# Kernel tuning notes

Hardware: AMD Instinct MI355X
Metric: run time of the kernel (lower is better)

## Reference

```python
import jax, jax.numpy as jnp
import numpy as np

NUM_HEADS = 12
TOP_K = 2
ROPE_THETA = 10000.0
EPS = 1e-6

def _rmsnorm(x, w):
    return x * jax.lax.rsqrt(jnp.mean(x * x, axis=-1, keepdims=True) + EPS) * w

def _rotate_half(t):
    t1, t2 = jnp.split(t, 2, axis=-1)
    return jnp.concatenate([-t2, t1], axis=-1)

def setup_inputs() -> dict:
    key = jax.random.key(0)
    ks = jax.random.split(key, 8)
    B, S, H, E, F = 2, 2048, 768, 8, 3072
    s = 0.02
    return {
        "x": jax.random.normal(ks[0], (B, S, H), dtype=jnp.float32),
        "attn_norm_w": jnp.ones((H,), dtype=jnp.float32),
        "wqkv": jax.random.normal(ks[1], (H, 3 * H), dtype=jnp.float32) * s,
        "wo": jax.random.normal(ks[2], (H, H), dtype=jnp.float32) * s,
        "ffn_norm_w": jnp.ones((H,), dtype=jnp.float32),
        "router_w": jax.random.normal(ks[3], (H, E), dtype=jnp.float32) * s,
        "w1": jax.random.normal(ks[4], (E, H, F), dtype=jnp.float32) * s,
        "w2": jax.random.normal(ks[5], (E, F, H), dtype=jnp.float32) * s,
    }

def reference(x, attn_norm_w, wqkv, wo, ffn_norm_w, router_w, w1, w2):
    B, S, H = x.shape
    NH, Dh = NUM_HEADS, H // NUM_HEADS
    E = router_w.shape[1]

    # ---- attention sub-block: x = x + attn(rmsnorm(x)) ----
    h = _rmsnorm(x, attn_norm_w)
    qkv = h @ wqkv  # (B,S,3H)
    q, k, v = [t.reshape(B, S, NH, Dh) for t in jnp.split(qkv, 3, axis=-1)]

    # RoPE (llama-style half-split rotation)
    half = Dh // 2
    inv_freq = 1.0 / (ROPE_THETA ** (jnp.arange(half, dtype=jnp.float32) / half))
    ang = jnp.arange(S, dtype=jnp.float32)[:, None] * inv_freq[None, :]  # (S, half)
    cos = jnp.concatenate([jnp.cos(ang)] * 2, axis=-1)[None, :, None, :].astype(x.dtype)
    sin = jnp.concatenate([jnp.sin(ang)] * 2, axis=-1)[None, :, None, :].astype(x.dtype)
    q = q * cos + _rotate_half(q) * sin
    k = k * cos + _rotate_half(k) * sin

    scores = jnp.einsum('bqhd,bkhd->bhqk', q, k) / jnp.sqrt(jnp.asarray(Dh, x.dtype))
    causal = jnp.tril(jnp.ones((S, S), dtype=bool))
    scores = jnp.where(causal[None, None], scores, jnp.asarray(-1e9, x.dtype))
    attn = jax.nn.softmax(scores, axis=-1)
    o = jnp.einsum('bhqk,bkhd->bqhd', attn, v).reshape(B, S, H) @ wo
    x = x + o

    # ---- MoE FFN sub-block: x = x + moe(rmsnorm(x)) ----
    hn = _rmsnorm(x, ffn_norm_w).reshape(-1, H)  # (T,H)
    logits = hn @ router_w  # (T,E)
    probs = jax.nn.softmax(logits, axis=-1)
    top_v, top_i = jax.lax.top_k(probs, TOP_K)  # (T,K)
    top_v = top_v / jnp.sum(top_v, axis=-1, keepdims=True)
    onehot = jax.nn.one_hot(top_i, E, dtype=x.dtype)  # (T,K,E)
    combine = jnp.einsum('tke,tk->te', onehot, top_v)  # (T,E)

    h1 = jnp.einsum('th,ehf->etf', hn, w1)
    h2 = jnp.einsum('etf,efh->eth', jax.nn.silu(h1), w2)
    moe_out = jnp.einsum('eth,te->th', h2, combine).reshape(B, S, H)

    # load-balancing aux loss (switch-style)
    frac = jnp.mean(jnp.sum(onehot, axis=1), axis=0) / TOP_K  # (E,)
    mean_prob = jnp.mean(probs, axis=0)  # (E,)
    aux = jnp.asarray(E, x.dtype) * jnp.sum(frac * mean_prob)

    return (x + moe_out, aux)
```

## Files before the change

kernel.cpp:

```cpp
#include <hip/hip_runtime.h>
#include <cstdint>
#include <cstddef>

typedef __bf16 bf16;
typedef bf16 bf16x8 __attribute__((ext_vector_type(8)));
typedef float f32x4 __attribute__((ext_vector_type(4)));

__device__ __forceinline__ void async_cp16(const void* g, void* l) {
    __builtin_amdgcn_global_load_lds(
        (const __attribute__((address_space(1))) unsigned int*)(unsigned long long)g,
        (__attribute__((address_space(3))) unsigned int*)(unsigned int)(unsigned long long)l,
        16, 0, 0);
}

__global__ __launch_bounds__(256) void transpose_cast(const float* __restrict__ in,
                                                      bf16* __restrict__ out, int R, int C) {
    __shared__ float tile[32][33];
    int bz = blockIdx.z;
    in  += (size_t)bz * R * C;
    out += (size_t)bz * R * C;
    int c0 = blockIdx.x * 32, r0 = blockIdx.y * 32;
    int tx = threadIdx.x & 31, ty = threadIdx.x >> 5;
#pragma unroll
    for (int i = 0; i < 4; ++i)
        tile[ty + i * 8][tx] = in[(size_t)(r0 + ty + i * 8) * C + c0 + tx];
    __syncthreads();
#pragma unroll
    for (int i = 0; i < 4; ++i)
        out[(size_t)(c0 + ty + i * 8) * R + r0 + tx] = (bf16)tile[tx][ty + i * 8];
}

__global__ __launch_bounds__(256) void rmsnorm_cast(const float* __restrict__ x,
                                                    const float* __restrict__ w,
                                                    bf16* __restrict__ out) {
    int row = blockIdx.x, tid = threadIdx.x;
    const float* xr = x + (size_t)row * 768;
    float v0 = xr[tid], v1 = xr[tid + 256], v2 = xr[tid + 512];
    float s = v0 * v0 + v1 * v1 + v2 * v2;
#pragma unroll
    for (int off = 32; off; off >>= 1) s += __shfl_xor(s, off, 64);
    __shared__ float red[4];
    if ((tid & 63) == 0) red[tid >> 6] = s;
    __syncthreads();
    float tot = red[0] + red[1] + red[2] + red[3];
    float rs = rsqrtf(tot * (1.f / 768.f) + 1e-6f);
    bf16* o = out + (size_t)row * 768;
    o[tid]       = (bf16)(v0 * rs * w[tid]);
    o[tid + 256] = (bf16)(v1 * rs * w[tid + 256]);
    o[tid + 512] = (bf16)(v2 * rs * w[tid + 512]);
}

__global__ __launch_bounds__(256) void rope_kernel(const bf16* __restrict__ qkv,
                                                   bf16* __restrict__ qb,
                                                   bf16* __restrict__ kb,
                                                   bf16* __restrict__ vtb) {
    __shared__ float vs[64][65];
    const int tid = threadIdx.x;
    const int s0 = blockIdx.x * 64, bh = blockIdx.y;
    const int b = bh / 12, h = bh - b * 12;
    const float qscale = 0.18033688f;
#pragma unroll
    for (int i = 0; i < 16; ++i) {
        int idx = i * 256 + tid;
        int sl = idx >> 6, d = idx & 63;
        int sg = s0 + sl;
        size_t base = ((size_t)b * 2048 + sg) * 2304;
        float qv = (float)qkv[base + h * 64 + d];
        float kv = (float)qkv[base + 768 + h * 64 + d];
        float vv = (float)qkv[base + 1536 + h * 64 + d];
        float qp = (float)qkv[base + h * 64 + (d ^ 32)];
        float kp = (float)qkv[base + 768 + h * 64 + (d ^ 32)];
        int jj = d & 31;
        float invf = __expf(-(float)jj * (9.210340371976184f / 32.f));
        float ang = (float)sg * invf;
        float cv, sv;
        __sincosf(ang, &sv, &cv);
        float rq = (d < 32) ? -qp : qp;
        float rk = (d < 32) ? -kp : kp;
        qb[((size_t)bh * 2048 + sg) * 64 + d] = (bf16)((qv * cv + rq * sv) * qscale);
        kb[((size_t)bh * 2048 + sg) * 64 + d] = (bf16)(kv * cv + rk * sv);
        vs[sl][d] = vv;
    }
    __syncthreads();
#pragma unroll
    for (int i = 0; i < 16; ++i) {
        int idx = i * 256 + tid;
        int d = idx >> 6, sl = idx & 63;
        vtb[(size_t)bh * 64 * 2048 + (size_t)d * 2048 + s0 + sl] = (bf16)vs[sl][d];
    }
}

__global__ __launch_bounds__(256) void attn_kernel(const bf16* __restrict__ qb,
                                                   const bf16* __restrict__ kb,
                                                   const bf16* __restrict__ vtb,
                                                   bf16* __restrict__ ob) {
    __shared__ __align__(16) bf16 Qs[2][64][32];
    __shared__ __align__(16) bf16 Ks[2][2][64][32];
    __shared__ __align__(16) bf16 Vts[2][2][64][32];
    __shared__ __align__(16) bf16 Ps[4][1024];

    const int tid = threadIdx.x, lane = tid & 63, w = tid >> 6;
    const int quad = lane >> 4, l16 = lane & 15;
    const int linear = (int)blockIdx.y * 32 + (int)blockIdx.x;
    const int xcd = linear & 7, j = linear >> 3;
    const int bh = xcd * 3 + (j >> 5);
    const int qt = 31 - (j & 31);
    const int q0 = qt * 64;
    const int b = bh / 12, h = bh - b * 12;

    const bf16* qhead = qb + (size_t)bh * 2048 * 64;
    const bf16* khead = kb + (size_t)bh * 2048 * 64;
    const bf16* vthead = vtb + (size_t)bh * 64 * 2048;

#pragma unroll
    for (int i = 0; i < 2; ++i) {
        int o = (i * 256 + tid) * 16;
        int kk = o >> 12, row = (o >> 6) & 63, el = (o & 63) >> 1;
        async_cp16(qhead + (size_t)(q0 + row) * 64 + kk * 32 + el,
                   (char*)Qs + (size_t)(i * 256 + w * 64) * 16);
    }
    __syncthreads();
    bf16x8 bq[2];
#pragma unroll
    for (int kk = 0; kk < 2; ++kk)
        bq[kk] = *(const bf16x8*)&Qs[kk][w * 16 + l16][quad * 8];

    f32x4 o_acc[4] = {};
    float m_st = -1e30f, l_st = 0.f;

    for (int j2 = 0; j2 <= qt; j2 += 2) {
        int nt2 = (j2 + 1 <= qt) ? 2 : 1;
        __syncthreads();
#pragma unroll
        for (int t = 0; t < 2; ++t) {
            if (t >= nt2) break;
            int kv0 = (j2 + t) * 64;
#pragma unroll
            for (int i = 0; i < 2; ++i) {
                int o = (i * 256 + tid) * 16;
                int kk = o >> 12, row = (o >> 6) & 63, el = (o & 63) >> 1;
                async_cp16(khead + (size_t)(kv0 + row) * 64 + kk * 32 + el,
                           (char*)&Ks[t] + (size_t)(i * 256 + w * 64) * 16);
                async_cp16(vthead + (size_t)row * 2048 + kv0 + kk * 32 + el,
                           (char*)&Vts[t] + (size_t)(i * 256 + w * 64) * 16);
            }
        }
        __syncthreads();

#pragma unroll
        for (int t = 0; t < 2; ++t) {
            if (t >= nt2) break;

            f32x4 sacc[4] = {};
#pragma unroll
            for (int kk = 0; kk < 2; ++kk) {
                bf16x8 ak[4];
#pragma unroll
                for (int ni = 0; ni < 4; ++ni)
                    ak[ni] = *(const bf16x8*)&Ks[t][kk][ni * 16 + l16][quad * 8];
#pragma unroll
                for (int ni = 0; ni < 4; ++ni)
                    sacc[ni] = __builtin_amdgcn_mfma_f32_16x16x32_bf16(ak[ni], bq[kk], sacc[ni], 0, 0, 0);
            }

            if (j2 + t == qt) {
                int ql = w * 16 + l16;
#pragma unroll
                for (int ni = 0; ni < 4; ++ni)
#pragma unroll
                    for (int r = 0; r < 4; ++r)
                        if (ni * 16 + quad * 4 + r > ql) sacc[ni][r] = -1e30f;
            }

            float mx = sacc[0][0];
#pragma unroll
            for (int ni = 0; ni < 4; ++ni)
#pragma unroll
                for (int r = 0; r < 4; ++r) mx = fmaxf(mx, sacc[ni][r]);
            mx = fmaxf(mx, __shfl_xor(mx, 16, 64));
            mx = fmaxf(mx, __shfl_xor(mx, 32, 64));
            float mnew = fmaxf(m_st, mx);
            float alpha = exp2f(m_st - mnew);
            m_st = mnew;
            float rsum = 0.f;
#pragma unroll
            for (int ni = 0; ni < 4; ++ni)
#pragma unroll
                for (int r = 0; r < 4; ++r) {
                    float pv = exp2f(sacc[ni][r] - mnew);
                    sacc[ni][r] = pv;
                    rsum += pv;
                }
            rsum += __shfl_xor(rsum, 16, 64);
            rsum += __shfl_xor(rsum, 32, 64);
            l_st = l_st * alpha + rsum;

            float af[4];
#pragma unroll
            for (int r = 0; r < 4; ++r) af[r] = __shfl(alpha, quad * 4 + r, 64);
#pragma unroll
            for (int ni = 0; ni < 4; ++ni)
#pragma unroll
                for (int r = 0; r < 4; ++r) o_acc[ni][r] *= af[r];

            bf16* pb = Ps[w];
#pragma unroll
            for (int ni = 0; ni < 4; ++ni)
#pragma unroll
                for (int r = 0; r < 4; ++r) {
                    int kv = ni * 16 + quad * 4 + r;
                    int ch = (kv >> 3) ^ (l16 & 7);
                    pb[l16 * 64 + ch * 8 + (kv & 7)] = (bf16)sacc[ni][r];
                }

#pragma unroll
            for (int kk = 0; kk < 2; ++kk) {
                int ch = (kk * 4 + quad) ^ (l16 & 7);
                bf16x8 ap = *(const bf16x8*)&pb[l16 * 64 + ch * 8];
                bf16x8 bv[4];
#pragma unroll
                for (int ni = 0; ni < 4; ++ni)
                    bv[ni] = *(const bf16x8*)&Vts[t][kk][ni * 16 + l16][quad * 8];
#pragma unroll
                for (int ni = 0; ni < 4; ++ni)
                    o_acc[ni] = __builtin_amdgcn_mfma_f32_16x16x32_bf16(ap, bv[ni], o_acc[ni], 0, 0, 0);
            }
        }
    }

    float lf[4];
#pragma unroll
    for (int r = 0; r < 4; ++r) lf[r] = 1.f / __shfl(l_st, quad * 4 + r, 64);
#pragma unroll
    for (int ni = 0; ni < 4; ++ni)
#pragma unroll
        for (int r = 0; r < 4; ++r) {
            int rowg = q0 + w * 16 + quad * 4 + r;
            size_t tk = (size_t)b * 2048 + rowg;
            ob[tk * 768 + h * 64 + ni * 16 + l16] = (bf16)(o_acc[ni][r] * lf[r]);
        }
}

__global__ __launch_bounds__(256) void rms_router(const float* __restrict__ x1,
                                                  const float* __restrict__ w,
                                                  const float* __restrict__ rw,
                                                  bf16* __restrict__ hn,
                                                  int* __restrict__ topi,
                                                  float* __restrict__ topw,
                                                  float* __restrict__ probsb) {
    __shared__ float hnf[768];
    __shared__ float part[256];
    __shared__ float lg[8];
    __shared__ float probs[8];
    __shared__ float red[4];
    int row = blockIdx.x, tid = threadIdx.x;
    const float* xr = x1 + (size_t)row * 768;
    float v0 = xr[tid], v1 = xr[tid + 256], v2 = xr[tid + 512];
    float s = v0 * v0 + v1 * v1 + v2 * v2;
#pragma unroll
    for (int off = 32; off; off >>= 1) s += __shfl_xor(s, off, 64);
    if ((tid & 63) == 0) red[tid >> 6] = s;
    __syncthreads();
    float tot = red[0] + red[1] + red[2] + red[3];
    float rs = rsqrtf(tot * (1.f / 768.f) + 1e-6f);
    float h0 = v0 * rs * w[tid], h1v = v1 * rs * w[tid + 256], h2v = v2 * rs * w[tid + 512];
    hnf[tid] = h0; hnf[tid + 256] = h1v; hnf[tid + 512] = h2v;
    bf16* o = hn + (size_t)row * 768;
    o[tid] = (bf16)h0; o[tid + 256] = (bf16)h1v; o[tid + 512] = (bf16)h2v;
    __syncthreads();
    int e = tid & 7, seg = tid >> 3;
    float p = 0.f;
#pragma unroll
    for (int j = 0; j < 24; ++j) { int k = seg * 24 + j; p += hnf[k] * rw[k * 8 + e]; }
    part[tid] = p;
    __syncthreads();
    if (tid < 8) { float a = 0.f; for (int sgi = 0; sgi < 32; ++sgi) a += part[sgi * 8 + tid]; lg[tid] = a; }
    __syncthreads();
    if (tid == 0) {
        float mx = lg[0];
        for (int i = 1; i < 8; ++i) mx = fmaxf(mx, lg[i]);
        float ssum = 0.f, ex[8];
        for (int i = 0; i < 8; ++i) { ex[i] = __expf(lg[i] - mx); ssum += ex[i]; }
        float inv = 1.f / ssum;
        for (int i = 0; i < 8; ++i) probs[i] = ex[i] * inv;
        int e0 = 0; float p0 = probs[0];
        for (int i = 1; i < 8; ++i) if (probs[i] > p0) { p0 = probs[i]; e0 = i; }
        int e1 = -1; float p1 = -1.f;
        for (int i = 0; i < 8; ++i) if (i != e0 && probs[i] > p1) { p1 = probs[i]; e1 = i; }
        float wsum = p0 + p1;
        topi[row * 2] = e0; topi[row * 2 + 1] = e1;
        topw[row * 2] = p0 / wsum; topw[row * 2 + 1] = p1 / wsum;
    }
    __syncthreads();
    if (tid < 8) probsb[(size_t)row * 8 + tid] = probs[tid];
}

__global__ __launch_bounds__(256) void router_stats(const float* __restrict__ probsb,
                                                    const int* __restrict__ topi,
                                                    int* ctrl, int4* tiles, float* auxOut) {
    __shared__ float pws[4][8];
    __shared__ int cws[4][8];
    int tid = threadIdx.x;
    float s[8] = {};
    int cnt[8] = {};
    for (int t = tid; t < 4096; t += 256) {
        const float4* p = (const float4*)(probsb + (size_t)t * 8);
        float4 a = p[0], b = p[1];
        s[0] += a.x; s[1] += a.y; s[2] += a.z; s[3] += a.w;
        s[4] += b.x; s[5] += b.y; s[6] += b.z; s[7] += b.w;
        int e0 = topi[2 * t], e1 = topi[2 * t + 1];
#pragma unroll
        for (int e = 0; e < 8; ++e) cnt[e] += (e == e0) + (e == e1);
    }
#pragma unroll
    for (int e = 0; e < 8; ++e)
#pragma unroll
        for (int off = 32; off; off >>= 1) {
            s[e] += __shfl_xor(s[e], off, 64);
            cnt[e] += __shfl_xor(cnt[e], off, 64);
        }
    if ((tid & 63) == 0) {
#pragma unroll
        for (int e = 0; e < 8; ++e) { pws[tid >> 6][e] = s[e]; cws[tid >> 6][e] = cnt[e]; }
    }
    __syncthreads();
    if (tid == 0) {
        int off = 0, nt = 0;
        float aux = 0.f;
        for (int e = 0; e < 8; ++e) {
            int ne = cws[0][e] + cws[1][e] + cws[2][e] + cws[3][e];
            float ps = pws[0][e] + pws[1][e] + pws[2][e] + pws[3][e];
            ctrl[e] = ne;
            ctrl[32 + e] = off;
            int ntl = (ne + 127) >> 7;
            for (int i = 0; i < ntl; ++i) { tiles[nt] = make_int4(e, off + i * 128, off + ne, 0); ++nt; }
            off += ntl << 7;
            aux += ((float)ne * (1.f / 8192.f)) * (ps * (1.f / 4096.f));
        }
        ctrl[24] = nt;
        auxOut[0] = 8.f * aux;
    }
}

__global__ __launch_bounds__(256) void place_tokens(const int* __restrict__ topi,
                                                    int* ctrl, int* __restrict__ perm,
                                                    int* __restrict__ tokslot) {
    __shared__ int lcnt[8], lbase[8];
    int tid = threadIdx.x;
    int t = blockIdx.x * 256 + tid;
    if (tid < 8) lcnt[tid] = 0;
    __syncthreads();
    int e0 = topi[2 * t], e1 = topi[2 * t + 1];
    int p0 = atomicAdd(&lcnt[e0], 1);
    int p1 = atomicAdd(&lcnt[e1], 1);
    __syncthreads();
    if (tid < 8) lbase[tid] = atomicAdd(&ctrl[16 + tid], lcnt[tid]);
    __syncthreads();
    int g0 = ctrl[32 + e0] + lbase[e0] + p0;
    int g1 = ctrl[32 + e1] + lbase[e1] + p1;
    perm[g0] = t; perm[g1] = t;
    tokslot[2 * t] = g0; tokslot[2 * t + 1] = g1;
}

__global__ __launch_bounds__(256) void moe_combine(const bf16* __restrict__ h2,
                                                   const int* __restrict__ tokslot,
                                                   const float* __restrict__ topw,
                                                   float* __restrict__ out) {
    int t = blockIdx.x, tid = threadIdx.x;
    int s0 = tokslot[2 * t], s1 = tokslot[2 * t + 1];
    float w0 = topw[2 * t], w1 = topw[2 * t + 1];
    const bf16* r0 = h2 + (size_t)s0 * 768;
    const bf16* r1 = h2 + (size_t)s1 * 768;
    float* o = out + (size_t)t * 768;
#pragma unroll
    for (int i = 0; i < 3; ++i) {
        int c = i * 256 + tid;
        o[c] += w0 * (float)r0[c] + w1 * (float)r1[c];
    }
}

template <int MODE, int NBX, int MTX>
__global__ __launch_bounds__(256) void gemm_nt(const bf16* __restrict__ A,
                                               const bf16* __restrict__ Bt,
                                               int N, int K,
                                               const float* __restrict__ xres,
                                               float* __restrict__ outF,
                                               bf16* __restrict__ outB,
                                               const int4* __restrict__ tiles,
                                               const int* __restrict__ ctrl,
                                               const int* __restrict__ perm) {
    __shared__ __align__(16) bf16 As[2][128 * 32];
    __shared__ __align__(16) bf16 Bs[2][128 * 32];
    __shared__ int sPerm[128];

    const int tid = threadIdx.x, lane = tid & 63, w = tid >> 6;
    const int wr = w >> 1, wc = w & 1, quad = lane >> 4, l16 = lane & 15;

    const int L = blockIdx.x;
    const int xcd = L & 7, j = L >> 3;
    const int mt = xcd * MTX + j / NBX;
    const int n0 = (j % NBX) * 128;

    int m0 = 0, row0 = 0;
    if (MODE <= 1) {
        m0 = mt * 128;
    } else {
        if (mt >= ctrl[24]) return;
        int4 td = tiles[mt];
        row0 = td.y;
        int rowend = td.z;
        Bt += (size_t)td.x * N * K;
        if (MODE == 2 && tid < 128) {
            int g = row0 + tid;
            int gs = (g < rowend) ? g : row0;
            sPerm[tid] = perm[gs];
        }
        if (MODE == 2) __syncthreads();
    }

    auto stage = [&](int buf, int kt) {
#pragma unroll
        for (int i = 0; i < 2; ++i) {
            int c = i * 256 + tid;
            int r = c >> 2, koff = (c & 3) * 8;
            const bf16* gp;
            if (MODE == 2)      gp = A + (size_t)sPerm[r] * K + kt + koff;
            else if (MODE == 3) gp = A + (size_t)(row0 + r) * K + kt + koff;
            else                gp = A + (size_t)(m0 + r) * K + kt + koff;
            async_cp16(gp, (char*)As[buf] + (size_t)(i * 256 + w * 64) * 16);
            async_cp16(Bt + (size_t)(n0 + r) * K + kt + koff,
                       (char*)Bs[buf] + (size_t)(i * 256 + w * 64) * 16);
        }
    };

    f32x4 acc[4][4] = {};
    const int nIt = K >> 5;
    stage(0, 0);

    for (int it = 0; it < nIt; ++it) {
        const int cur = it & 1;
        __syncthreads();
        if (it + 1 < nIt) stage(cur ^ 1, (it + 1) << 5);

        bf16x8 af[4], bfr[4];
#pragma unroll
        for (int mi = 0; mi < 4; ++mi)
            af[mi] = *(const bf16x8*)(As[cur] + (wr * 64 + mi * 16 + l16) * 32 + quad * 8);
#pragma unroll
        for (int ni = 0; ni < 4; ++ni)
            bfr[ni] = *(const bf16x8*)(Bs[cur] + (wc * 64 + ni * 16 + l16) * 32 + quad * 8);
#pragma unroll
        for (int mi = 0; mi < 4; ++mi)
#pragma unroll
            for (int ni = 0; ni < 4; ++ni)
                acc[mi][ni] = __builtin_amdgcn_mfma_f32_16x16x32_bf16(af[mi], bfr[ni], acc[mi][ni], 0, 0, 0);
    }

#pragma unroll
    for (int mi = 0; mi < 4; ++mi)
#pragma unroll
        for (int ni = 0; ni < 4; ++ni)
#pragma unroll
            for (int r = 0; r < 4; ++r) {
                int lrow = wr * 64 + mi * 16 + quad * 4 + r;
                int col = n0 + wc * 64 + ni * 16 + l16;
                float v = acc[mi][ni][r];
                if (MODE == 0) {
                    outB[(size_t)(m0 + lrow) * N + col] = (bf16)v;
                } else if (MODE == 1) {
                    size_t idx = (size_t)(m0 + lrow) * N + col;
                    outF[idx] = v + xres[idx];
                } else if (MODE == 2) {
                    float sv = v / (1.f + __expf(-v));
                    outB[(size_t)(row0 + lrow) * N + col] = (bf16)sv;
                } else {
                    outB[(size_t)(row0 + lrow) * N + col] = (bf16)v;
                }
            }
}

__global__ void zero_ctrl(int* ctrl) { if (threadIdx.x < 64) ctrl[threadIdx.x] = 0; }

extern "C" void kernel_launch(void* const* d_in, const int* in_sizes, int n_in,
                              void* d_out, int out_size, void* d_ws, size_t ws_size,
                              hipStream_t stream) {
    const float* x    = (const float*)d_in[0];
    const float* anw  = (const float*)d_in[1];
    const float* wqkv = (const float*)d_in[2];
    const float* wo   = (const float*)d_in[3];
    const float* fnw  = (const float*)d_in[4];
    const float* rw   = (const float*)d_in[5];
    const float* w1   = (const float*)d_in[6];
    const float* w2   = (const float*)d_in[7];
    float* out = (float*)d_out;

    char* ws = (char*)d_ws;
    size_t off = 0;
    auto alloc = [&](size_t bytes) -> char* {
        char* p = ws + off;
        off = (off + bytes + 255) & ~(size_t)255;
        return p;
    };
    bf16* wqkvT = (bf16*)alloc(2304ull * 768 * 2);
    bf16* woT   = (bf16*)alloc(768ull * 768 * 2);
    bf16* w1T   = (bf16*)alloc(8ull * 3072 * 768 * 2);
    bf16* w2T   = (bf16*)alloc(8ull * 768 * 3072 * 2);
    bf16* hbuf  = (bf16*)alloc(4096ull * 768 * 2);
    bf16* qkvb  = (bf16*)alloc(4096ull * 2304 * 2);
    bf16* qb    = (bf16*)alloc(24ull * 2048 * 64 * 2);
    bf16* kb    = (bf16*)alloc(24ull * 2048 * 64 * 2);
    bf16* vtb   = (bf16*)alloc(24ull * 64 * 2048 * 2);
    bf16* obuf  = (bf16*)alloc(4096ull * 768 * 2);
    bf16* hn    = (bf16*)alloc(4096ull * 768 * 2);
    int*  topi  = (int*)alloc(4096ull * 2 * 4);
    float* topw = (float*)alloc(4096ull * 2 * 4);
    float* probsb = (float*)alloc(4096ull * 8 * 4);
    int*  ctrl  = (int*)alloc(64 * 4);
    int4* tiles = (int4*)alloc(80 * 16);
    int*  perm  = (int*)alloc(9216 * 4);
    int*  tokslot = (int*)alloc(4096ull * 2 * 4);
    bf16* h1    = (bf16*)alloc(9216ull * 3072 * 2);
    bf16* h2    = qkvb;
    (void)ws_size; (void)in_sizes; (void)n_in;

    zero_ctrl<<<1, 64, 0, stream>>>(ctrl);
    transpose_cast<<<dim3(72, 24, 1), 256, 0, stream>>>(wqkv, wqkvT, 768, 2304);
    transpose_cast<<<dim3(24, 24, 1), 256, 0, stream>>>(wo, woT, 768, 768);
    transpose_cast<<<dim3(96, 24, 8), 256, 0, stream>>>(w1, w1T, 768, 3072);
    transpose_cast<<<dim3(24, 96, 8), 256, 0, stream>>>(w2, w2T, 3072, 768);
    rmsnorm_cast<<<4096, 256, 0, stream>>>(x, anw, hbuf);
    gemm_nt<0, 18, 4><<<576, 256, 0, stream>>>(hbuf, wqkvT, 2304, 768,
                                               nullptr, nullptr, qkvb, nullptr, nullptr, nullptr);
    rope_kernel<<<dim3(32, 24), 256, 0, stream>>>(qkvb, qb, kb, vtb);
    attn_kernel<<<dim3(32, 24), 256, 0, stream>>>(qb, kb, vtb, obuf);
    gemm_nt<1, 6, 4><<<192, 256, 0, stream>>>(obuf, woT, 768, 768,
                                              x, out, nullptr, nullptr, nullptr, nullptr);
    rms_router<<<4096, 256, 0, stream>>>(out, fnw, rw, hn, topi, topw, probsb);
    router_stats<<<1, 256, 0, stream>>>(probsb, topi, ctrl, tiles, out + (out_size - 1));
    place_tokens<<<16, 256, 0, stream>>>(topi, ctrl, perm, tokslot);
    gemm_nt<2, 24, 9><<<1728, 256, 0, stream>>>(hn, w1T, 3072, 768,
                                                nullptr, nullptr, h1, tiles, ctrl, perm);
    gemm_nt<3, 6, 9><<<432, 256, 0, stream>>>(h1, w2T, 768, 3072,
                                              nullptr, nullptr, h2, tiles, ctrl, perm);
    moe_combine<<<4096, 256, 0, stream>>>(h2, tokslot, topw, out);
}
```

Measured before the change: 499.9 us.

## Add 256x256 eight-wave pipelined GEMM for QKV and MoE up-projection

Adds a new gemm8p kernel with 512 threads, 256x256 output tiles, 64-wide K stages with XOR-swizzled LDS, and a phased schedule that overlaps async global-to-LDS copies with MFMA quadrants using explicit waitcnt, barriers and setprio. It replaces the QKV projection and the MoE w1 GEMM, so expert token groups are now padded to 256 rows, and the w2 GEMM maps two 128-row halves onto each 256-row tile. The larger tiles are meant to raise arithmetic intensity and MFMA utilisation, at the cost of more padding waste per expert, larger buffers and lower occupancy.

```diff
diff --git a/kernel.cpp b/kernel.cpp
--- a/kernel.cpp
+++ b/kernel.cpp
@@ -12,6 +12,11 @@
         (__attribute__((address_space(3))) unsigned int*)(unsigned int)(unsigned long long)l,
         16, 0, 0);
 }
+
+#define BARX() __builtin_amdgcn_s_barrier()
+#define LGKM0() asm volatile("s_waitcnt lgkmcnt(0)" ::: "memory")
+#define VMC4() asm volatile("s_waitcnt vmcnt(4)" ::: "memory")
+#define VMC0() asm volatile("s_waitcnt vmcnt(0)" ::: "memory")
 
 __global__ __launch_bounds__(256) void transpose_cast(const float* __restrict__ in,
                                                       bf16* __restrict__ out, int R, int C) {
@@ -332,9 +337,9 @@
             float ps = pws[0][e] + pws[1][e] + pws[2][e] + pws[3][e];
             ctrl[e] = ne;
             ctrl[32 + e] = off;
-            int ntl = (ne + 127) >> 7;
-            for (int i = 0; i < ntl; ++i) { tiles[nt] = make_int4(e, off + i * 128, off + ne, 0); ++nt; }
-            off += ntl << 7;
+            int ntl = (ne + 255) >> 8;
+            for (int i = 0; i < ntl; ++i) { tiles[nt] = make_int4(e, off + i * 256, off + ne, 0); ++nt; }
+            off += ntl << 8;
             aux += ((float)ne * (1.f / 8192.f)) * (ps * (1.f / 4096.f));
         }
         ctrl[24] = nt;
@@ -377,6 +382,183 @@
         int c = i * 256 + tid;
         o[c] += w0 * (float)r0[c] + w1 * (float)r1[c];
     }
+}
+
+template <int MODE>
+__global__ __launch_bounds__(512, 2) void gemm8p(const bf16* __restrict__ A,
+                                                 const bf16* __restrict__ Bt,
+                                                 int N, int K,
+                                                 bf16* __restrict__ outB,
+                                                 const int4* __restrict__ tiles,
+                                                 const int* __restrict__ ctrl,
+                                                 const int* __restrict__ perm) {
+    __shared__ __align__(16) bf16 As[2][2][128 * 64];
+    __shared__ __align__(16) bf16 Bs[2][2][128 * 64];
+    __shared__ int sPerm[256];
+
+    const int tid = threadIdx.x, lane = tid & 63, wid = tid >> 6;
+    const int wr = wid >> 2, wc = wid & 3;
+    const int quad = lane >> 4, l16 = lane & 15;
+
+    const int NB = N >> 8;
+    const int mt = (int)blockIdx.x / NB;
+    const int n0 = ((int)blockIdx.x % NB) << 8;
+
+    int m0 = 0, row0 = 0;
+    if (MODE == 0) {
+        m0 = mt << 8;
+    } else {
+        if (mt >= ctrl[24]) return;
+        int4 td = tiles[mt];
+        row0 = td.y;
+        Bt += (size_t)td.x * (size_t)N * K;
+        if (tid < 256) {
+            int g = row0 + tid;
+            sPerm[tid] = perm[(g < td.z) ? g : row0];
+        }
+        __syncthreads();
+    }
+
+    const int r0t = tid >> 3;
+    const int s0t = tid & 7;
+    const int cOff = ((s0t ^ (r0t & 7)) << 3);
+    const bf16* pA[2][2];
+    const bf16* pB[2][2];
+#pragma unroll
+    for (int h = 0; h < 2; ++h)
+#pragma unroll
+        for (int i = 0; i < 2; ++i) {
+            int rrow = h * 128 + i * 64 + r0t;
+            pB[h][i] = Bt + (size_t)(n0 + rrow) * K + cOff;
+            if (MODE == 0) pA[h][i] = A + (size_t)(m0 + rrow) * K + cOff;
+            else           pA[h][i] = A + (size_t)sPerm[rrow] * K + cOff;
+        }
+
+    auto stA = [&](int buf, int h, int kt) {
+#pragma unroll
+        for (int i = 0; i < 2; ++i)
+            async_cp16(pA[h][i] + kt, (char*)As[buf][h] + (size_t)((i * 512 + wid * 64) * 16));
+    };
+    auto stB = [&](int buf, int h, int kt) {
+#pragma unroll
+        for (int i = 0; i < 2; ++i)
+            async_cp16(pB[h][i] + kt, (char*)Bs[buf][h] + (size_t)((i * 512 + wid * 64) * 16));
+    };
+    auto ldA = [&](int buf, int mi, int kk) -> bf16x8 {
+        int r = mi * 16 + l16;
+        int s = (kk * 4 + quad) ^ (l16 & 7);
+        return *(const bf16x8*)((const char*)As[buf][wr] + r * 128 + s * 16);
+    };
+    auto ldB = [&](int buf, int ni, int kk) -> bf16x8 {
+        int c = wc * 64 + ni * 16 + l16;
+        int s = (kk * 4 + quad) ^ (l16 & 7);
+        return *(const bf16x8*)((const char*)Bs[buf][c >> 7] + (c & 127) * 128 + s * 16);
+    };
+
+    f32x4 acc[8][4] = {};
+    bf16x8 aLo[4][2], aHi[4][2], bLo[2][2], bHi[2][2];
+
+    auto ktile = [&](int b, auto S1, auto S2, auto S3, auto S4, int vm) {
+#pragma unroll
+        for (int mi = 0; mi < 4; ++mi) { aLo[mi][0] = ldA(b, mi, 0); aLo[mi][1] = ldA(b, mi, 1); }
+#pragma unroll
+        for (int ni = 0; ni < 2; ++ni) { bLo[ni][0] = ldB(b, ni, 0); bLo[ni][1] = ldB(b, ni, 1); }
+        S1();
+        BARX(); LGKM0();
+        __builtin_amdgcn_s_setprio(1);
+#pragma unroll
+        for (int mi = 0; mi < 4; ++mi)
+#pragma unroll
+            for (int ni = 0; ni < 2; ++ni) {
+                acc[mi][ni] = __builtin_amdgcn_mfma_f32_16x16x32_bf16(aLo[mi][0], bLo[ni][0], acc[mi][ni], 0, 0, 0);
+                acc[mi][ni] = __builtin_amdgcn_mfma_f32_16x16x32_bf16(aLo[mi][1], bLo[ni][1], acc[mi][ni], 0, 0, 0);
+            }
+        __builtin_amdgcn_s_setprio(0);
+        BARX();
+#pragma unroll
+        for (int ni = 0; ni < 2; ++ni) { bHi[ni][0] = ldB(b, ni + 2, 0); bHi[ni][1] = ldB(b, ni + 2, 1); }
+        S2();
+        BARX(); LGKM0();
+        __builtin_amdgcn_s_setprio(1);
+#pragma unroll
+        for (int mi = 0; mi < 4; ++mi)
+#pragma unroll
+            for (int ni = 0; ni < 2; ++ni) {
+                acc[mi][ni + 2] = __builtin_amdgcn_mfma_f32_16x16x32_bf16(aLo[mi][0], bHi[ni][0], acc[mi][ni + 2], 0, 0, 0);
+                acc[mi][ni + 2] = __builtin_amdgcn_mfma_f32_16x16x32_bf16(aLo[mi][1], bHi[ni][1], acc[mi][ni + 2], 0, 0, 0);
+            }
+        __builtin_amdgcn_s_setprio(0);
+        BARX();
+#pragma unroll
+        for (int mi = 0; mi < 4; ++mi) { aHi[mi][0] = ldA(b, mi + 4, 0); aHi[mi][1] = ldA(b, mi + 4, 1); }
+        S3();
+        BARX(); LGKM0();
+        __builtin_amdgcn_s_setprio(1);
+#pragma unroll
+        for (int mi = 0; mi < 4; ++mi)
+#pragma unroll
+            for (int ni = 0; ni < 2; ++ni) {
+                acc[mi + 4][ni + 2] = __builtin_amdgcn_mfma_f32_16x16x32_bf16(aHi[mi][0], bHi[ni][0], acc[mi + 4][ni + 2], 0, 0, 0);
+                acc[mi + 4][ni + 2] = __builtin_amdgcn_mfma_f32_16x16x32_bf16(aHi[mi][1], bHi[ni][1], acc[mi + 4][ni + 2], 0, 0, 0);
+            }
+        __builtin_amdgcn_s_setprio(0);
+        BARX();
+        S4();
+        BARX(); LGKM0();
+        __builtin_amdgcn_s_setprio(1);
+#pragma unroll
+        for (int mi = 0; mi < 4; ++mi)
+#pragma unroll
+            for (int ni = 0; ni < 2; ++ni) {
+                acc[mi + 4][ni] = __builtin_amdgcn_mfma_f32_16x16x32_bf16(aHi[mi][0], bLo[ni][0], acc[mi + 4][ni], 0, 0, 0);
+                acc[mi + 4][ni] = __builtin_amdgcn_mfma_f32_16x16x32_bf16(aHi[mi][1], bLo[ni][1], acc[mi + 4][ni], 0, 0, 0);
+            }
+        __builtin_amdgcn_s_setprio(0);
+        if (vm == 4) { VMC4(); } else if (vm == 0) { VMC0(); }
+        BARX();
+    };
+
+    stA(0, 0, 0); stA(0, 1, 0); stB(0, 0, 0); stB(0, 1, 0);
+    stB(1, 0, 64); stB(1, 1, 64);
+    VMC4();
+    BARX();
+
+    const int nIt = K >> 7;
+    for (int it = 0; it < nIt; ++it) {
+        const bool last = (it == nIt - 1);
+        const int kA = (it * 2 + 1) << 6;
+        const int kB = (it * 2 + 2) << 6;
+        const int kC = (it * 2 + 3) << 6;
+        ktile(0,
+              [&] { stA(1, 0, kA); },
+              [&] { stA(1, 1, kA); },
+              [&] { if (!last) stB(0, 0, kB); },
+              [&] { if (!last) stB(0, 1, kB); },
+              last ? 0 : 4);
+        ktile(1,
+              [&] { if (!last) stA(0, 0, kB); },
+              [&] { if (!last) stA(0, 1, kB); },
+              [&] { if (!last) stB(1, 0, kC); },
+              [&] { if (!last) stB(1, 1, kC); },
+              last ? -1 : 4);
+    }
+
+#pragma unroll
+    for (int mi = 0; mi < 8; ++mi)
+#pragma unroll
+        for (int ni = 0; ni < 4; ++ni)
+#pragma unroll
+            for (int r = 0; r < 4; ++r) {
+                int lrow = wr * 128 + mi * 16 + quad * 4 + r;
+                int col  = n0 + wc * 64 + ni * 16 + l16;
+                float v = acc[mi][ni][r];
+                if (MODE == 0) {
+                    outB[(size_t)(m0 + lrow) * N + col] = (bf16)v;
+                } else {
+                    float sv = v / (1.f + __expf(-v));
+                    outB[(size_t)(row0 + lrow) * N + col] = (bf16)sv;
+                }
+            }
 }
 
 template <int MODE, int NBX, int MTX>
@@ -404,18 +586,24 @@
     int m0 = 0, row0 = 0;
     if (MODE <= 1) {
         m0 = mt * 128;
-    } else {
+    } else if (MODE == 2) {
         if (mt >= ctrl[24]) return;
         int4 td = tiles[mt];
         row0 = td.y;
         int rowend = td.z;
         Bt += (size_t)td.x * N * K;
-        if (MODE == 2 && tid < 128) {
+        if (tid < 128) {
             int g = row0 + tid;
             int gs = (g < rowend) ? g : row0;
             sPerm[tid] = perm[gs];
         }
-        if (MODE == 2) __syncthreads();
+        __syncthreads();
+    } else {
+        int tt = mt >> 1;
+        if (tt >= ctrl[24]) return;
+        int4 td = tiles[tt];
+        row0 = td.y + ((mt & 1) << 7);
+        Bt += (size_t)td.x * N * K;
     }
 
     auto stage = [&](int buf, int kt) {
@@ -517,9 +705,9 @@
     float* probsb = (float*)alloc(4096ull * 8 * 4);
     int*  ctrl  = (int*)alloc(64 * 4);
     int4* tiles = (int4*)alloc(80 * 16);
-    int*  perm  = (int*)alloc(9216 * 4);
+    int*  perm  = (int*)alloc(10240 * 4);
     int*  tokslot = (int*)alloc(4096ull * 2 * 4);
-    bf16* h1    = (bf16*)alloc(9216ull * 3072 * 2);
+    bf16* h1    = (bf16*)alloc(10240ull * 3072 * 2);
     bf16* h2    = qkvb;
     (void)ws_size; (void)in_sizes; (void)n_in;
 
@@ -529,8 +717,7 @@
     transpose_cast<<<dim3(96, 24, 8), 256, 0, stream>>>(w1, w1T, 768, 3072);
     transpose_cast<<<dim3(24, 96, 8), 256, 0, stream>>>(w2, w2T, 3072, 768);
     rmsnorm_cast<<<4096, 256, 0, stream>>>(x, anw, hbuf);
-    gemm_nt<0, 18, 4><<<576, 256, 0, stream>>>(hbuf, wqkvT, 2304, 768,
-                                               nullptr, nullptr, qkvb, nullptr, nullptr, nullptr);
+    gemm8p<0><<<144, 512, 0, stream>>>(hbuf, wqkvT, 2304, 768, qkvb, nullptr, nullptr, nullptr);
     rope_kernel<<<dim3(32, 24), 256, 0, stream>>>(qkvb, qb, kb, vtb);
     attn_kernel<<<dim3(32, 24), 256, 0, stream>>>(qb, kb, vtb, obuf);
     gemm_nt<1, 6, 4><<<192, 256, 0, stream>>>(obuf, woT, 768, 768,
@@ -538,9 +725,8 @@
     rms_router<<<4096, 256, 0, stream>>>(out, fnw, rw, hn, topi, topw, probsb);
     router_stats<<<1, 256, 0, stream>>>(probsb, topi, ctrl, tiles, out + (out_size - 1));
     place_tokens<<<16, 256, 0, stream>>>(topi, ctrl, perm, tokslot);
-    gemm_nt<2, 24, 9><<<1728, 256, 0, stream>>>(hn, w1T, 3072, 768,
-                                                nullptr, nullptr, h1, tiles, ctrl, perm);
-    gemm_nt<3, 6, 9><<<432, 256, 0, stream>>>(h1, w2T, 768, 3072,
-                                              nullptr, nullptr, h2, tiles, ctrl, perm);
+    gemm8p<2><<<480, 512, 0, stream>>>(hn, w1T, 3072, 768, h1, tiles, ctrl, perm);
+    gemm_nt<3, 6, 10><<<480, 256, 0, stream>>>(h1, w2T, 768, 3072,
+                                               nullptr, nullptr, h2, tiles, ctrl, perm);
     moe_combine<<<4096, 256, 0, stream>>>(h2, tokslot, topw, out);
 }
```

After: 500.4 us. Within noise of the previous version (+0.1%).
